# Performance work log

Measured on AMD Instinct MI355X. Metric: run time of the kernel, lower is better.

The kernel has to match this reference:

```python
import jax, jax.numpy as jnp
import numpy as np

N = 100000          # num nodes
E = 1_600_000       # num edges
D = 128             # in_channels
H = 128             # hidden_channels
NUM_LAYERS = 3


def setup_inputs() -> dict:
    key = jax.random.key(0)
    ks = jax.random.split(key, 6)
    return {
        "emb": jax.random.normal(ks[0], (N, D), dtype=jnp.float32),
        "w1": jax.random.normal(ks[1], (H, D), dtype=jnp.float32) / np.sqrt(D).astype(np.float32),
        "b1": jnp.zeros((H,), jnp.float32),
        "w2": jax.random.normal(ks[2], (H, H), dtype=jnp.float32) / np.sqrt(H).astype(np.float32),
        "b2": jnp.zeros((H,), jnp.float32),
        "eps": jnp.zeros((NUM_LAYERS,), jnp.float32),  # learn_eps=True, init 0 per layer
        "edge_w": jax.random.uniform(ks[3], (E,), dtype=jnp.float32),
        "src": jax.random.randint(ks[4], (E,), 0, N, dtype=jnp.int32),
        "dst": jax.random.randint(ks[5], (E,), 0, N, dtype=jnp.int32),
    }


def _gin_layer(x, src, dst, edge_w, deg_inv, eps, W, b):
    # DGL GINConv(mean, edge_weight): msg = x[src] * w ; agg = mean over in-edges (divide by in-degree)
    msg = x[src] * edge_w[:, None]                                  # [E, d]
    agg = jax.ops.segment_sum(msg, dst, num_segments=N) * deg_inv[:, None]
    return ((1.0 + eps) * x + agg) @ W.T + b


def reference(emb, w1, b1, w2, b2, eps, edge_w, src, dst):
    # in-degree (count of in-edges), zero-degree nodes get 0 aggregation
    deg = jax.ops.segment_sum(jnp.ones((E,), jnp.float32), dst, num_segments=N)
    deg_inv = jnp.where(deg > 0, 1.0 / jnp.maximum(deg, 1.0), 0.0)

    x = _gin_layer(emb, src, dst, edge_w, deg_inv, eps[0], w1, b1)
    x = jax.nn.relu(x)  # dropout is identity in eval mode
    for i in range(1, NUM_LAYERS - 1):
        x = _gin_layer(x, src, dst, edge_w, deg_inv, eps[i], w2, b2)  # lin2 shared
        x = jax.nn.relu(x)
    x = _gin_layer(x, src, dst, edge_w, deg_inv, eps[NUM_LAYERS - 1], w2, b2)
    x = x.at[0].set(jnp.zeros((x.shape[1],), x.dtype))  # x[0] = zeros
    return x
```

## Files before the change

### kernel.cpp

```cpp
#include <hip/hip_runtime.h>
#include <hip/hip_bf16.h>

#define N_NODES 100000
#define N_EDGES 1600000
#define DIM 128
#define SCAN_CHUNK 1024

typedef __attribute__((ext_vector_type(8))) short bf16x8;
typedef __attribute__((ext_vector_type(4))) float f32x4;
typedef __attribute__((ext_vector_type(4))) short bf16x4;

__device__ __forceinline__ float b2f(short s) {
    return __uint_as_float(((unsigned int)(unsigned short)s) << 16);
}

__global__ void cvtall_kernel(const float* __restrict__ emb, const float* __restrict__ w1,
                              const float* __restrict__ w2, __hip_bfloat16* __restrict__ embb,
                              __hip_bfloat16* __restrict__ w1b, __hip_bfloat16* __restrict__ w2b) {
    const int n4e = N_NODES * DIM / 4;
    const int n4w = DIM * DIM / 4;
    int i = blockIdx.x * blockDim.x + threadIdx.x;
    const float* in;
    __hip_bfloat16* out;
    int j;
    if (i < n4e) { in = emb; out = embb; j = i; }
    else if (i < n4e + n4w) { in = w1; out = w1b; j = i - n4e; }
    else if (i < n4e + 2 * n4w) { in = w2; out = w2b; j = i - n4e - n4w; }
    else return;
    f32x4 v = ((const f32x4*)in)[j];
    bf16x4 o;
    o.x = (short)__bfloat16_as_ushort(__float2bfloat16(v.x));
    o.y = (short)__bfloat16_as_ushort(__float2bfloat16(v.y));
    o.z = (short)__bfloat16_as_ushort(__float2bfloat16(v.z));
    o.w = (short)__bfloat16_as_ushort(__float2bfloat16(v.w));
    ((bf16x4*)out)[j] = o;
}

__global__ __launch_bounds__(256) void degrank_kernel(const int* __restrict__ dst,
                                                      int* __restrict__ deg,
                                                      int* __restrict__ rank) {
    const int S = 2048 * 256;
    int tid = blockIdx.x * blockDim.x + threadIdx.x;
    int e3 = tid + 3 * S;
    int d0 = dst[tid];
    int d1 = dst[tid + S];
    int d2 = dst[tid + 2 * S];
    int d3 = (e3 < N_EDGES) ? dst[e3] : -1;
    int r0 = atomicAdd(&deg[d0], 1);
    int r1 = atomicAdd(&deg[d1], 1);
    int r2 = atomicAdd(&deg[d2], 1);
    int r3 = (d3 >= 0) ? atomicAdd(&deg[d3], 1) : 0;
    rank[tid] = r0;
    rank[tid + S] = r1;
    rank[tid + 2 * S] = r2;
    if (e3 < N_EDGES) rank[e3] = r3;
}

__global__ void scan1_kernel(const int* __restrict__ deg, int* __restrict__ bsum) {
    __shared__ int s[256];
    int t = threadIdx.x;
    int base = blockIdx.x * SCAN_CHUNK + t * 4;
    int v = 0;
    for (int k = 0; k < 4; k++) { int i = base + k; if (i < N_NODES) v += deg[i]; }
    s[t] = v;
    __syncthreads();
    for (int off = 128; off > 0; off >>= 1) { if (t < off) s[t] += s[t + off]; __syncthreads(); }
    if (t == 0) bsum[blockIdx.x] = s[0];
}

__global__ void scan2_kernel(const int* __restrict__ bsum, int* __restrict__ bscan,
                             int* __restrict__ row_start, int nb) {
    if (threadIdx.x == 0) {
        int run = 0;
        for (int b = 0; b < nb; b++) { bscan[b] = run; run += bsum[b]; }
        row_start[N_NODES] = run;
    }
}

__global__ void scan3_kernel(const int* __restrict__ deg, const int* __restrict__ bscan,
                             int* __restrict__ row_start) {
    __shared__ int s[256];
    int t = threadIdx.x;
    int base = blockIdx.x * SCAN_CHUNK + t * 4;
    int v[4]; int tot = 0;
    for (int k = 0; k < 4; k++) { int i = base + k; v[k] = (i < N_NODES) ? deg[i] : 0; tot += v[k]; }
    s[t] = tot;
    __syncthreads();
    for (int off = 1; off < 256; off <<= 1) {
        int a = (t >= off) ? s[t - off] : 0;
        __syncthreads();
        s[t] += a;
        __syncthreads();
    }
    int run = s[t] - tot + bscan[blockIdx.x];
    for (int k = 0; k < 4; k++) {
        int i = base + k;
        if (i < N_NODES) row_start[i] = run;
        run += v[k];
    }
}

#define FI_UNROLL 4
__global__ void fill_kernel(const int* __restrict__ src, const int* __restrict__ dst,
                            const float* __restrict__ ew, const int* __restrict__ rank,
                            const int* __restrict__ row_start, int2* __restrict__ sw_s) {
    int tid = blockIdx.x * blockDim.x + threadIdx.x;
    int nthreads = gridDim.x * blockDim.x;
    int d_[FI_UNROLL], r_[FI_UNROLL], s_[FI_UNROLL], w_[FI_UNROLL], rs_[FI_UNROLL];
#pragma unroll
    for (int k = 0; k < FI_UNROLL; k++) {
        int e = tid + k * nthreads;
        if (e < N_EDGES) {
            d_[k] = dst[e]; r_[k] = rank[e]; s_[k] = src[e] << 8; w_[k] = __float_as_int(ew[e]);
        } else d_[k] = -1;
    }
#pragma unroll
    for (int k = 0; k < FI_UNROLL; k++)
        if (d_[k] >= 0) rs_[k] = row_start[d_[k]];
#pragma unroll
    for (int k = 0; k < FI_UNROLL; k++)
        if (d_[k] >= 0) sw_s[rs_[k] + r_[k]] = make_int2(s_[k], w_[k]);
}

template <int RELU, int ZERO0, int OUTBF>
__global__ __launch_bounds__(256) void aggmm_kernel(const __hip_bfloat16* __restrict__ x,
                                                    const int* __restrict__ row_start,
                                                    const int2* __restrict__ sw_s,
                                                    const float* __restrict__ eps, int li,
                                                    const __hip_bfloat16* __restrict__ W,
                                                    const float* __restrict__ bias,
                                                    void* __restrict__ outv) {
    __shared__ int2 s_sw[4][4][64];
    __shared__ __hip_bfloat162 s_h[16][64];
    int wv = threadIdx.x >> 6;
    int lane = threadIdx.x & 63;
    int row0 = blockIdx.x * 16;
    int c = lane & 31;
    int half = lane >> 5;
    const char* xb = (const char*)x + (c << 3);
    float ep = 1.0f + eps[li];

    int n0 = row0 + wv * 4;
    int beg[4], cnt[4];
#pragma unroll
    for (int j = 0; j < 4; j++) {
        beg[j] = row_start[n0 + j];
        cnt[j] = row_start[n0 + j + 1] - beg[j];
    }

    bf16x4 xs[4];
#pragma unroll
    for (int j = 0; j < 4; j++)
        xs[j] = *(const bf16x4*)((const char*)x + (size_t)(n0 + j) * 256 + (c << 3));
    int2 er[4];
#pragma unroll
    for (int j = 0; j < 4; j++) {
        er[j] = make_int2(0, 0);
        if (lane < cnt[j]) er[j] = sw_s[beg[j] + lane];
    }
#pragma unroll
    for (int j = 0; j < 4; j++) s_sw[wv][j][lane] = er[j];
    asm volatile("s_waitcnt lgkmcnt(0)" ::: "memory");

    float acc[4][4] = {};
    int cmax = max(max(cnt[0], cnt[1]), max(cnt[2], cnt[3]));
    int c0 = min(cmax, 64);
    int c02 = (c0 + 1) & ~1;
#pragma unroll 2
    for (int i = 0; i < c02; i += 2) {
#pragma unroll
        for (int j = 0; j < 4; j++) {
            int2 e = s_sw[wv][j][i + half];
            bf16x4 v = *(const bf16x4*)(xb + e.x);
            float w = __int_as_float(e.y);
            acc[j][0] += b2f(v.x) * w;
            acc[j][1] += b2f(v.y) * w;
            acc[j][2] += b2f(v.z) * w;
            acc[j][3] += b2f(v.w) * w;
        }
    }
    asm volatile("" ::: "memory");

    if (cmax > 64) {
#pragma unroll 1
        for (int j = 0; j < 4; j++) {
            int nd = cnt[j];
#pragma unroll 1
            for (int base = 64; base < nd; base += 64) {
                int cc = min(64, nd - base);
                int2 er2 = make_int2(0, 0);
                if (lane < cc) er2 = sw_s[beg[j] + base + lane];
                s_sw[wv][j][lane] = er2;
                asm volatile("s_waitcnt lgkmcnt(0)" ::: "memory");
                int cc2 = (cc + 1) & ~1;
                for (int i = 0; i < cc2; i += 2) {
                    int2 e = s_sw[wv][j][i + half];
                    bf16x4 v = *(const bf16x4*)(xb + e.x);
                    float w = __int_as_float(e.y);
                    acc[j][0] += b2f(v.x) * w;
                    acc[j][1] += b2f(v.y) * w;
                    acc[j][2] += b2f(v.z) * w;
                    acc[j][3] += b2f(v.w) * w;
                }
                asm volatile("" ::: "memory");
            }
        }
    }

#pragma unroll
    for (int j = 0; j < 4; j++) {
        float a0 = acc[j][0] + __shfl_xor(acc[j][0], 32, 64);
        float a1 = acc[j][1] + __shfl_xor(acc[j][1], 32, 64);
        float a2 = acc[j][2] + __shfl_xor(acc[j][2], 32, 64);
        float a3 = acc[j][3] + __shfl_xor(acc[j][3], 32, 64);
        if (half == 0) {
            float dinv = cnt[j] > 0 ? 1.0f / (float)cnt[j] : 0.0f;
            bf16x4 o;
            o.x = (short)__bfloat16_as_ushort(__float2bfloat16(ep * b2f(xs[j].x) + a0 * dinv));
            o.y = (short)__bfloat16_as_ushort(__float2bfloat16(ep * b2f(xs[j].y) + a1 * dinv));
            o.z = (short)__bfloat16_as_ushort(__float2bfloat16(ep * b2f(xs[j].z) + a2 * dinv));
            o.w = (short)__bfloat16_as_ushort(__float2bfloat16(ep * b2f(xs[j].w) + a3 * dinv));
            int jr = wv * 4 + j;
            int co = (c * 8) ^ ((jr & 7) << 4);
            *(bf16x4*)((char*)&s_h[jr][0] + co) = o;
        }
    }
    __syncthreads();

    int lr = lane & 15;
    int kg = lane >> 4;
    bf16x8 a[4];
#pragma unroll
    for (int k = 0; k < 4; k++) {
        int cb = (kg * 16 + k * 64) ^ ((lr & 7) << 4);
        a[k] = *(const bf16x8*)((const char*)&s_h[lr][0] + cb);
    }
    __syncthreads();

    f32x4 accm[2];
#pragma unroll
    for (int t = 0; t < 2; t++) {
        int jt = wv * 2 + t;
        const short* Wp = (const short*)W + (size_t)(jt * 16 + lr) * DIM + kg * 8;
        f32x4 cc = {0.f, 0.f, 0.f, 0.f};
#pragma unroll
        for (int k = 0; k < 4; k++) {
            bf16x8 b = *(const bf16x8*)(Wp + k * 32);
            cc = __builtin_amdgcn_mfma_f32_16x16x32_bf16(a[k], b, cc, 0, 0, 0);
        }
        accm[t] = cc;
    }

    int colb = lane & 15;
    int rb = (lane >> 4) * 4;
    if (OUTBF) {
#pragma unroll
        for (int t = 0; t < 2; t++) {
            int col = (wv * 2 + t) * 16 + colb;
            float bv = bias[col];
#pragma unroll
            for (int r = 0; r < 4; r++) {
                int row = rb + r;
                float v = accm[t][r] + bv;
                if (RELU) v = fmaxf(v, 0.f);
                if (ZERO0 && blockIdx.x == 0 && row == 0) v = 0.f;
                int bo = (row * 256 + col * 2) ^ ((row & 7) << 4);
                *(__hip_bfloat16*)((char*)s_h + bo) = __float2bfloat16(v);
            }
        }
        __syncthreads();
        int row = threadIdx.x >> 4, c16 = threadIdx.x & 15;
        int bo = (row * 256 + c16 * 16) ^ ((row & 7) << 4);
        bf16x8 vv = *(const bf16x8*)((const char*)s_h + bo);
        *(bf16x8*)((char*)outv + (size_t)(row0 + row) * 256 + c16 * 16) = vv;
    } else {
#pragma unroll
        for (int t = 0; t < 2; t++) {
            int col = (wv * 2 + t) * 16 + colb;
            float bv = bias[col];
#pragma unroll
            for (int r = 0; r < 4; r++) {
                int grow = row0 + rb + r;
                float v = accm[t][r] + bv;
                if (RELU) v = fmaxf(v, 0.f);
                if (ZERO0 && grow == 0) v = 0.f;
                ((float*)outv)[(size_t)grow * DIM + col] = v;
            }
        }
    }
}

extern "C" void kernel_launch(void* const* d_in, const int* in_sizes, int n_in,
                              void* d_out, int out_size, void* d_ws, size_t ws_size,
                              hipStream_t stream) {
    const float* emb = (const float*)d_in[0];
    const float* w1  = (const float*)d_in[1];
    const float* b1  = (const float*)d_in[2];
    const float* w2  = (const float*)d_in[3];
    const float* b2  = (const float*)d_in[4];
    const float* eps = (const float*)d_in[5];
    const float* ew  = (const float*)d_in[6];
    const int* src   = (const int*)d_in[7];
    const int* dst   = (const int*)d_in[8];
    float* out = (float*)d_out;

    char* base = (char*)d_ws;
    size_t off = 0;
    auto alloc = [&](size_t bytes) -> char* {
        char* p = base + off;
        off += (bytes + 255) & ~(size_t)255;
        return p;
    };
    int* deg            = (int*)alloc((size_t)N_NODES * 4);
    int* row_start      = (int*)alloc((size_t)(N_NODES + 1) * 4);
    int* rank           = (int*)alloc((size_t)N_EDGES * 4);
    int* bsum           = (int*)alloc(128 * 4);
    int* bscan          = (int*)alloc(128 * 4);
    int2* sw_s          = (int2*)alloc((size_t)N_EDGES * 8);
    __hip_bfloat16* xb  = (__hip_bfloat16*)alloc((size_t)N_NODES * DIM * 2);
    __hip_bfloat16* xc  = (__hip_bfloat16*)alloc((size_t)N_NODES * DIM * 2);
    __hip_bfloat16* embb= (__hip_bfloat16*)alloc((size_t)N_NODES * DIM * 2);
    __hip_bfloat16* w1b = (__hip_bfloat16*)alloc(DIM * DIM * 2);
    __hip_bfloat16* w2b = (__hip_bfloat16*)alloc(DIM * DIM * 2);

    hipMemsetAsync(deg, 0, (size_t)N_NODES * 4, stream);

    {
        int n4 = N_NODES * DIM / 4 + 2 * (DIM * DIM / 4);
        cvtall_kernel<<<(n4 + 255) / 256, 256, 0, stream>>>(emb, w1, w2, embb, w1b, w2b);
    }

    degrank_kernel<<<2048, 256, 0, stream>>>(dst, deg, rank);
    int nb = (N_NODES + SCAN_CHUNK - 1) / SCAN_CHUNK;
    scan1_kernel<<<nb, 256, 0, stream>>>(deg, bsum);
    scan2_kernel<<<1, 64, 0, stream>>>(bsum, bscan, row_start, nb);
    scan3_kernel<<<nb, 256, 0, stream>>>(deg, bscan, row_start);
    {
        int nthreads = ((N_EDGES + FI_UNROLL - 1) / FI_UNROLL + 255) & ~255;
        fill_kernel<<<nthreads / 256, 256, 0, stream>>>(src, dst, ew, rank, row_start, sw_s);
    }

    int blocks = N_NODES / 16;
    aggmm_kernel<1, 0, 1><<<blocks, 256, 0, stream>>>(embb, row_start, sw_s, eps, 0, w1b, b1, xb);
    aggmm_kernel<1, 0, 1><<<blocks, 256, 0, stream>>>(xb,   row_start, sw_s, eps, 1, w2b, b2, xc);
    aggmm_kernel<0, 1, 0><<<blocks, 256, 0, stream>>>(xc,   row_start, sw_s, eps, 2, w2b, b2, out);
}
```

Baseline: 458.7 us.

## Widen gather to 16-byte bf16x8 loads and fuse degree with conversion kernel

The aggregation gather now has each lane load 8 bf16 values (16 bytes) per edge, with four edges in flight per wavefront instead of two. Partial sums are reduced with two xor-shuffles, and the self-feature load moves into the epilogue. The degree/rank kernel and the fp32-to-bf16 conversion kernel are merged into one launch to save a launch and let the two run concurrently. Launch bounds now request 4 blocks per SM; the 8-wide accumulators raise register pressure, and the extra shuffle adds reduction cost.

```diff
diff --git a/kernel.cpp b/kernel.cpp
--- a/kernel.cpp
+++ b/kernel.cpp
@@ -14,46 +14,50 @@
     return __uint_as_float(((unsigned int)(unsigned short)s) << 16);
 }
 
-__global__ void cvtall_kernel(const float* __restrict__ emb, const float* __restrict__ w1,
-                              const float* __restrict__ w2, __hip_bfloat16* __restrict__ embb,
-                              __hip_bfloat16* __restrict__ w1b, __hip_bfloat16* __restrict__ w2b) {
-    const int n4e = N_NODES * DIM / 4;
-    const int n4w = DIM * DIM / 4;
-    int i = blockIdx.x * blockDim.x + threadIdx.x;
-    const float* in;
-    __hip_bfloat16* out;
-    int j;
-    if (i < n4e) { in = emb; out = embb; j = i; }
-    else if (i < n4e + n4w) { in = w1; out = w1b; j = i - n4e; }
-    else if (i < n4e + 2 * n4w) { in = w2; out = w2b; j = i - n4e - n4w; }
-    else return;
-    f32x4 v = ((const f32x4*)in)[j];
-    bf16x4 o;
-    o.x = (short)__bfloat16_as_ushort(__float2bfloat16(v.x));
-    o.y = (short)__bfloat16_as_ushort(__float2bfloat16(v.y));
-    o.z = (short)__bfloat16_as_ushort(__float2bfloat16(v.z));
-    o.w = (short)__bfloat16_as_ushort(__float2bfloat16(v.w));
-    ((bf16x4*)out)[j] = o;
-}
-
-__global__ __launch_bounds__(256) void degrank_kernel(const int* __restrict__ dst,
-                                                      int* __restrict__ deg,
-                                                      int* __restrict__ rank) {
-    const int S = 2048 * 256;
-    int tid = blockIdx.x * blockDim.x + threadIdx.x;
-    int e3 = tid + 3 * S;
-    int d0 = dst[tid];
-    int d1 = dst[tid + S];
-    int d2 = dst[tid + 2 * S];
-    int d3 = (e3 < N_EDGES) ? dst[e3] : -1;
-    int r0 = atomicAdd(&deg[d0], 1);
-    int r1 = atomicAdd(&deg[d1], 1);
-    int r2 = atomicAdd(&deg[d2], 1);
-    int r3 = (d3 >= 0) ? atomicAdd(&deg[d3], 1) : 0;
-    rank[tid] = r0;
-    rank[tid + S] = r1;
-    rank[tid + 2 * S] = r2;
-    if (e3 < N_EDGES) rank[e3] = r3;
+__global__ __launch_bounds__(256) void degcvt_kernel(const int* __restrict__ dst,
+                                                     int* __restrict__ deg,
+                                                     int* __restrict__ rank,
+                                                     const float* __restrict__ emb,
+                                                     const float* __restrict__ w1,
+                                                     const float* __restrict__ w2,
+                                                     __hip_bfloat16* __restrict__ embb,
+                                                     __hip_bfloat16* __restrict__ w1b,
+                                                     __hip_bfloat16* __restrict__ w2b) {
+    if (blockIdx.x < 2048) {
+        const int S = 2048 * 256;
+        int tid = blockIdx.x * blockDim.x + threadIdx.x;
+        int e3 = tid + 3 * S;
+        int d0 = dst[tid];
+        int d1 = dst[tid + S];
+        int d2 = dst[tid + 2 * S];
+        int d3 = (e3 < N_EDGES) ? dst[e3] : -1;
+        int r0 = atomicAdd(&deg[d0], 1);
+        int r1 = atomicAdd(&deg[d1], 1);
+        int r2 = atomicAdd(&deg[d2], 1);
+        int r3 = (d3 >= 0) ? atomicAdd(&deg[d3], 1) : 0;
+        rank[tid] = r0;
+        rank[tid + S] = r1;
+        rank[tid + 2 * S] = r2;
+        if (e3 < N_EDGES) rank[e3] = r3;
+    } else {
+        const int n4e = N_NODES * DIM / 4;
+        const int n4w = DIM * DIM / 4;
+        int i = (blockIdx.x - 2048) * blockDim.x + threadIdx.x;
+        const float* in;
+        __hip_bfloat16* out;
+        int j;
+        if (i < n4e) { in = emb; out = embb; j = i; }
+        else if (i < n4e + n4w) { in = w1; out = w1b; j = i - n4e; }
+        else if (i < n4e + 2 * n4w) { in = w2; out = w2b; j = i - n4e - n4w; }
+        else return;
+        f32x4 v = ((const f32x4*)in)[j];
+        bf16x4 o;
+        o.x = (short)__bfloat16_as_ushort(__float2bfloat16(v.x));
+        o.y = (short)__bfloat16_as_ushort(__float2bfloat16(v.y));
+        o.z = (short)__bfloat16_as_ushort(__float2bfloat16(v.z));
+        o.w = (short)__bfloat16_as_ushort(__float2bfloat16(v.w));
+        ((bf16x4*)out)[j] = o;
+    }
 }
 
 __global__ void scan1_kernel(const int* __restrict__ deg, int* __restrict__ bsum) {
@@ -123,21 +127,21 @@
 }
 
 template <int RELU, int ZERO0, int OUTBF>
-__global__ __launch_bounds__(256) void aggmm_kernel(const __hip_bfloat16* __restrict__ x,
-                                                    const int* __restrict__ row_start,
-                                                    const int2* __restrict__ sw_s,
-                                                    const float* __restrict__ eps, int li,
-                                                    const __hip_bfloat16* __restrict__ W,
-                                                    const float* __restrict__ bias,
-                                                    void* __restrict__ outv) {
+__global__ __launch_bounds__(256, 4) void aggmm_kernel(const __hip_bfloat16* __restrict__ x,
+                                                       const int* __restrict__ row_start,
+                                                       const int2* __restrict__ sw_s,
+                                                       const float* __restrict__ eps, int li,
+                                                       const __hip_bfloat16* __restrict__ W,
+                                                       const float* __restrict__ bias,
+                                                       void* __restrict__ outv) {
     __shared__ int2 s_sw[4][4][64];
     __shared__ __hip_bfloat162 s_h[16][64];
     int wv = threadIdx.x >> 6;
     int lane = threadIdx.x & 63;
     int row0 = blockIdx.x * 16;
-    int c = lane & 31;
-    int half = lane >> 5;
-    const char* xb = (const char*)x + (c << 3);
+    int c16 = lane & 15;
+    int q = lane >> 4;
+    const char* xb = (const char*)x + (c16 << 4);
     float ep = 1.0f + eps[li];
 
     int n0 = row0 + wv * 4;
@@ -148,10 +152,6 @@
         cnt[j] = row_start[n0 + j + 1] - beg[j];
     }
 
-    bf16x4 xs[4];
-#pragma unroll
-    for (int j = 0; j < 4; j++)
-        xs[j] = *(const bf16x4*)((const char*)x + (size_t)(n0 + j) * 256 + (c << 3));
     int2 er[4];
 #pragma unroll
     for (int j = 0; j < 4; j++) {
@@ -162,21 +162,18 @@
     for (int j = 0; j < 4; j++) s_sw[wv][j][lane] = er[j];
     asm volatile("s_waitcnt lgkmcnt(0)" ::: "memory");
 
-    float acc[4][4] = {};
+    float acc[4][8] = {};
     int cmax = max(max(cnt[0], cnt[1]), max(cnt[2], cnt[3]));
-    int c0 = min(cmax, 64);
-    int c02 = (c0 + 1) & ~1;
+    int c04 = (min(cmax, 64) + 3) & ~3;
 #pragma unroll 2
-    for (int i = 0; i < c02; i += 2) {
+    for (int i = 0; i < c04; i += 4) {
 #pragma unroll
         for (int j = 0; j < 4; j++) {
-            int2 e = s_sw[wv][j][i + half];
-            bf16x4 v = *(const bf16x4*)(xb + e.x);
+            int2 e = s_sw[wv][j][i + q];
+            bf16x8 v = *(const bf16x8*)(xb + e.x);
             float w = __int_as_float(e.y);
-            acc[j][0] += b2f(v.x) * w;
-            acc[j][1] += b2f(v.y) * w;
-            acc[j][2] += b2f(v.z) * w;
-            acc[j][3] += b2f(v.w) * w;
+#pragma unroll
+            for (int k = 0; k < 8; k++) acc[j][k] += b2f(v[k]) * w;
         }
     }
     asm volatile("" ::: "memory");
@@ -192,15 +189,13 @@
                 if (lane < cc) er2 = sw_s[beg[j] + base + lane];
                 s_sw[wv][j][lane] = er2;
                 asm volatile("s_waitcnt lgkmcnt(0)" ::: "memory");
-                int cc2 = (cc + 1) & ~1;
-                for (int i = 0; i < cc2; i += 2) {
-                    int2 e = s_sw[wv][j][i + half];
-                    bf16x4 v = *(const bf16x4*)(xb + e.x);
+                int cc4 = (cc + 3) & ~3;
+                for (int i = 0; i < cc4; i += 4) {
+                    int2 e = s_sw[wv][j][i + q];
+                    bf16x8 v = *(const bf16x8*)(xb + e.x);
                     float w = __int_as_float(e.y);
-                    acc[j][0] += b2f(v.x) * w;
-                    acc[j][1] += b2f(v.y) * w;
-                    acc[j][2] += b2f(v.z) * w;
-                    acc[j][3] += b2f(v.w) * w;
+#pragma unroll
+                    for (int k = 0; k < 8; k++) acc[j][k] += b2f(v[k]) * w;
                 }
                 asm volatile("" ::: "memory");
             }
@@ -209,20 +204,25 @@
 
 #pragma unroll
     for (int j = 0; j < 4; j++) {
-        float a0 = acc[j][0] + __shfl_xor(acc[j][0], 32, 64);
-        float a1 = acc[j][1] + __shfl_xor(acc[j][1], 32, 64);
-        float a2 = acc[j][2] + __shfl_xor(acc[j][2], 32, 64);
-        float a3 = acc[j][3] + __shfl_xor(acc[j][3], 32, 64);
-        if (half == 0) {
+        float a[8];
+#pragma unroll
+        for (int k = 0; k < 8; k++) {
+            float t = acc[j][k];
+            t += __shfl_xor(t, 16, 64);
+            t += __shfl_xor(t, 32, 64);
+            a[k] = t;
+        }
+        if (q == 0) {
             float dinv = cnt[j] > 0 ? 1.0f / (float)cnt[j] : 0.0f;
-            bf16x4 o;
-            o.x = (short)__bfloat16_as_ushort(__float2bfloat16(ep * b2f(xs[j].x) + a0 * dinv));
-            o.y = (short)__bfloat16_as_ushort(__float2bfloat16(ep * b2f(xs[j].y) + a1 * dinv));
-            o.z = (short)__bfloat16_as_ushort(__float2bfloat16(ep * b2f(xs[j].z) + a2 * dinv));
-            o.w = (short)__bfloat16_as_ushort(__float2bfloat16(ep * b2f(xs[j].w) + a3 * dinv));
+            bf16x8 xs = *(const bf16x8*)((const char*)x + (size_t)(n0 + j) * 256 + (c16 << 4));
+            bf16x8 o;
+#pragma unroll
+            for (int k = 0; k < 8; k++)
+                o[k] = (short)__bfloat16_as_ushort(
+                    __float2bfloat16(ep * b2f(xs[k]) + a[k] * dinv));
             int jr = wv * 4 + j;
-            int co = (c * 8) ^ ((jr & 7) << 4);
-            *(bf16x4*)((char*)&s_h[jr][0] + co) = o;
+            int co = (c16 << 4) ^ ((jr & 7) << 4);
+            *(bf16x8*)((char*)&s_h[jr][0] + co) = o;
         }
     }
     __syncthreads();
@@ -269,10 +269,10 @@
             }
         }
         __syncthreads();
-        int row = threadIdx.x >> 4, c16 = threadIdx.x & 15;
-        int bo = (row * 256 + c16 * 16) ^ ((row & 7) << 4);
+        int row = threadIdx.x >> 4, cc16 = threadIdx.x & 15;
+        int bo = (row * 256 + cc16 * 16) ^ ((row & 7) << 4);
         bf16x8 vv = *(const bf16x8*)((const char*)s_h + bo);
-        *(bf16x8*)((char*)outv + (size_t)(row0 + row) * 256 + c16 * 16) = vv;
+        *(bf16x8*)((char*)outv + (size_t)(row0 + row) * 256 + cc16 * 16) = vv;
     } else {
 #pragma unroll
         for (int t = 0; t < 2; t++) {
@@ -327,10 +327,11 @@
 
     {
         int n4 = N_NODES * DIM / 4 + 2 * (DIM * DIM / 4);
-        cvtall_kernel<<<(n4 + 255) / 256, 256, 0, stream>>>(emb, w1, w2, embb, w1b, w2b);
-    }
-
-    degrank_kernel<<<2048, 256, 0, stream>>>(dst, deg, rank);
+        int cvtb = (n4 + 255) / 256;
+        degcvt_kernel<<<2048 + cvtb, 256, 0, stream>>>(dst, deg, rank, emb, w1, w2,
+                                                       embb, w1b, w2b);
+    }
+
     int nb = (N_NODES + SCAN_CHUNK - 1) / SCAN_CHUNK;
     scan1_kernel<<<nb, 256, 0, stream>>>(deg, bsum);
     scan2_kernel<<<1, 64, 0, stream>>>(bsum, bscan, row_start, nb);
```

Result: slower. 490.5 us (+6.9%).
